# Kernel tuning notes

Measured on AMD Instinct MI355X. Metric: run time of the kernel, lower is better.

The kernel has to match this reference:

```python
import jax, jax.numpy as jnp
import numpy as np

H, KV, D, HID, FF = 32, 8, 128, 4096, 14336
EPS = 1e-5
ROPE_THETA = 1e9


def setup_inputs() -> dict:
    key = jax.random.key(0)
    ks = jax.random.split(key, 10)
    B, S = 1, 2048
    s = 0.02
    return {
        "hidden_states": jax.random.normal(ks[0], (B, S, HID), dtype=jnp.float32),
        "wq": jax.random.normal(ks[1], (HID, H * D), dtype=jnp.float32) * s,
        "wk": jax.random.normal(ks[2], (HID, KV * D), dtype=jnp.float32) * s,
        "wv": jax.random.normal(ks[3], (HID, KV * D), dtype=jnp.float32) * s,
        "wo": jax.random.normal(ks[4], (H * D, HID), dtype=jnp.float32) * s,
        "w_gate": jax.random.normal(ks[5], (HID, FF), dtype=jnp.float32) * s,
        "w_up": jax.random.normal(ks[6], (HID, FF), dtype=jnp.float32) * s,
        "w_down": jax.random.normal(ks[7], (FF, HID), dtype=jnp.float32) * s,
        "ln1_w": jnp.ones((HID,), dtype=jnp.float32),
        "ln2_w": jnp.ones((HID,), dtype=jnp.float32),
        "position_ids": jnp.arange(B * S, dtype=jnp.int32).reshape(B, S),
    }


def _rmsnorm(x, w):
    var = jnp.mean(jnp.square(x), axis=-1, keepdims=True)
    return x * jax.lax.rsqrt(var + EPS) * w


def _rope_cos_sin(position_ids):
    inv_freq = 1.0 / (ROPE_THETA ** (jnp.arange(0, D, 2, dtype=jnp.float32) / D))  # [D/2]
    ang = position_ids.astype(jnp.float32)[..., None] * inv_freq  # [B,S,D/2]
    ang = jnp.concatenate([ang, ang], axis=-1)  # [B,S,D]
    return jnp.cos(ang), jnp.sin(ang)


def _rotate_half(x):
    x1, x2 = x[..., : D // 2], x[..., D // 2:]
    return jnp.concatenate([-x2, x1], axis=-1)


def _apply_rope(x, cos, sin):
    # x: [B,S,h,D]; cos/sin: [B,S,D]
    c, s = cos[:, :, None, :], sin[:, :, None, :]
    return x * c + _rotate_half(x) * s


def reference(hidden_states, wq, wk, wv, wo, w_gate, w_up, w_down, ln1_w, ln2_w, position_ids):
    B, S, _ = hidden_states.shape
    G = H // KV  # query groups per kv head

    # --- attention block ---
    residual = hidden_states
    x = _rmsnorm(hidden_states, ln1_w)
    q = (x @ wq).reshape(B, S, H, D)
    k = (x @ wk).reshape(B, S, KV, D)
    v = (x @ wv).reshape(B, S, KV, D)

    cos, sin = _rope_cos_sin(position_ids)
    q = _apply_rope(q, cos, sin)
    k = _apply_rope(k, cos, sin)

    # GQA: group query heads over kv heads, [B,S,KV,G,D]
    qg = q.reshape(B, S, KV, G, D)
    scores = jnp.einsum("bqhgd,bkhd->bhgqk", qg, k) / jnp.sqrt(jnp.float32(D))
    causal = position_ids[:, :, None] >= position_ids[:, None, :]  # [B,S,S]
    scores = jnp.where(causal[:, None, None, :, :], scores, jnp.float32(-1e9))
    probs = jax.nn.softmax(scores, axis=-1)
    attn = jnp.einsum("bhgqk,bkhd->bqhgd", probs, v).reshape(B, S, H * D)
    hidden_states = residual + attn @ wo

    # --- MLP block (SwiGLU) ---
    residual = hidden_states
    x = _rmsnorm(hidden_states, ln2_w)
    mlp = (jax.nn.silu(x @ w_gate) * (x @ w_up)) @ w_down
    return residual + mlp
```

## Files before the change

kernel.cpp:

```cpp
#include <hip/hip_runtime.h>

typedef short bf16x8 __attribute__((ext_vector_type(8)));
typedef float f32x4 __attribute__((ext_vector_type(4)));

#define DEV __device__ __forceinline__

constexpr int SEQ = 2048;
constexpr int HID = 4096;
constexpr int NH  = 32;
constexpr int NKV = 8;
constexpr int DH  = 128;
constexpr int FF  = 14336;
constexpr int QKVN = NH * DH + 2 * NKV * DH;

DEV unsigned short f2bf(float f) {
  union { float f; unsigned u; } x; x.f = f;
  unsigned r = x.u + 0x7fffu + ((x.u >> 16) & 1u);
  return (unsigned short)(r >> 16);
}
DEV float bf2f(unsigned short u) {
  union { unsigned u; float f; } x; x.u = ((unsigned)u) << 16; return x.f;
}
DEV void gload16(const void* g, void* l) {
  __builtin_amdgcn_global_load_lds(
      (const __attribute__((address_space(1))) unsigned*)g,
      (__attribute__((address_space(3))) unsigned*)l, 16, 0, 0);
}

__global__ __launch_bounds__(256) void rmsnorm_kernel(
    const float* __restrict__ x, const float* __restrict__ w,
    unsigned short* __restrict__ out) {
  const int row = blockIdx.x;
  const int tid = threadIdx.x;
  const float* xr = x + (size_t)row * HID;
  float4 v[4];
  float ss = 0.f;
#pragma unroll
  for (int i = 0; i < 4; ++i) {
    v[i] = *(const float4*)(xr + i * 1024 + tid * 4);
    ss += v[i].x * v[i].x + v[i].y * v[i].y + v[i].z * v[i].z + v[i].w * v[i].w;
  }
#pragma unroll
  for (int m = 1; m < 64; m <<= 1) ss += __shfl_xor(ss, m);
  __shared__ float red[4];
  if ((tid & 63) == 0) red[tid >> 6] = ss;
  __syncthreads();
  float tot = red[0] + red[1] + red[2] + red[3];
  float rms = rsqrtf(tot / (float)HID + 1e-5f);
  unsigned short* orow = out + (size_t)row * HID;
#pragma unroll
  for (int i = 0; i < 4; ++i) {
    int base = i * 1024 + tid * 4;
    ushort4 o;
    o.x = f2bf(v[i].x * rms * w[base + 0]);
    o.y = f2bf(v[i].y * rms * w[base + 1]);
    o.z = f2bf(v[i].z * rms * w[base + 2]);
    o.w = f2bf(v[i].w * rms * w[base + 3]);
    *(ushort4*)(orow + base) = o;
  }
}

__global__ __launch_bounds__(256) void wtrans_kernel(
    const float* __restrict__ W, unsigned short* __restrict__ WT, int K,
    int N) {
  __shared__ unsigned short t[64][72];
  const int k0 = blockIdx.x * 64, n0 = blockIdx.y * 64;
  const int tid = threadIdx.x;
  const int tk = tid >> 4;
  const int tn4 = (tid & 15) * 4;
#pragma unroll
  for (int p = 0; p < 4; ++p) {
    int k = tk + p * 16;
    float4 v = *(const float4*)(W + (size_t)(k0 + k) * N + n0 + tn4);
    t[tn4 + 0][k] = f2bf(v.x);
    t[tn4 + 1][k] = f2bf(v.y);
    t[tn4 + 2][k] = f2bf(v.z);
    t[tn4 + 3][k] = f2bf(v.w);
  }
  __syncthreads();
#pragma unroll
  for (int p = 0; p < 4; ++p) {
    int n = tk + p * 16;
    ushort4 o = *(const ushort4*)&t[n][tn4];
    *(ushort4*)(WT + (size_t)(n0 + n) * K + k0 + tn4) = o;
  }
}

__global__ __launch_bounds__(256) void rope_kernel(unsigned short* __restrict__ x,
                                                   int nheads, int ld) {
  const int gid = blockIdx.x * 256 + threadIdx.x;
  const int i = gid & 63;
  const int t = gid >> 6;
  const int s = t / nheads;
  const int hh = t - s * nheads;
  float ang = (float)s * exp2f((float)i * (-29.897352853986263f / 64.f));
  float sn, cs;
  sincosf(ang, &sn, &cs);
  size_t base = (size_t)s * ld + hh * DH + i;
  float x1 = bf2f(x[base]);
  float x2 = bf2f(x[base + 64]);
  x[base]      = f2bf(x1 * cs - x2 * sn);
  x[base + 64] = f2bf(x2 * cs + x1 * sn);
}

__global__ __launch_bounds__(256) void silu_mul_kernel(
    const unsigned short* __restrict__ g, const unsigned short* __restrict__ u,
    unsigned short* __restrict__ out) {
  const size_t idx = ((size_t)blockIdx.x * 256 + threadIdx.x) * 4;
  ushort4 gv = *(const ushort4*)(g + idx);
  ushort4 uv = *(const ushort4*)(u + idx);
  float gf[4] = {bf2f(gv.x), bf2f(gv.y), bf2f(gv.z), bf2f(gv.w)};
  float uf[4] = {bf2f(uv.x), bf2f(uv.y), bf2f(uv.z), bf2f(uv.w)};
  ushort4 o;
  unsigned short* op = (unsigned short*)&o;
#pragma unroll
  for (int j = 0; j < 4; ++j) {
    float sl = gf[j] / (1.f + __expf(-gf[j]));
    op[j] = f2bf(sl * uf[j]);
  }
  *(ushort4*)(out + idx) = o;
}

template <int WROWS, int EPI>
__global__ __launch_bounds__(512, 2) void gemm8p_kernel(
    const unsigned short* __restrict__ A, const unsigned short* __restrict__ BT,
    void* __restrict__ Cv, const float* __restrict__ res, int gridM, int N,
    int K) {
  constexpr int BM = 2 * WROWS;
  constexpr int MF = WROWS / 32;
  constexpr int H  = 2 + BM / 128;
  constexpr int ABYTES = BM * 128;
  constexpr int BUFBYTES = ABYTES + 32768;
  __shared__ __align__(128) char sm[2 * BUFBYTES];

  const int tid  = threadIdx.x;
  const int lane = tid & 63;
  const int wv   = tid >> 6;
  const int nwg = gridDim.x;
  const int b = blockIdx.x;
  const int logical = (b & 7) * (nwg >> 3) + (b >> 3);
  const int m0 = (logical % gridM) * BM;
  const int n0 = (logical / gridM) * 256;
  const int wm = (wv >> 2) * WROWS;
  const int wn = (wv & 3) * 64;
  const int nt = K >> 6;

  const int srow = tid >> 3;
  const int scolb = (tid & 7) * 16;
  const int sldsbase = wv * 1024;

  auto stage = [&](int h, int t) {
    const int buf = t & 1;
    const int kt = t * 64;
    char* ldsOp;
    const unsigned short* g;
    int grow0, rowBase;
    if (h < 2) {
      ldsOp = sm + buf * BUFBYTES + ABYTES; g = BT; grow0 = n0; rowBase = h * 128;
    } else {
      ldsOp = sm + buf * BUFBYTES;          g = A;  grow0 = m0; rowBase = (h - 2) * 128;
    }
#pragma unroll
    for (int r = 0; r < 2; ++r) {
      int row = rowBase + r * 64 + srow;
      const char* gp = (const char*)g + ((size_t)(grow0 + row) * K + kt) * 2 +
                       (scolb ^ ((row & 7) << 4));
      gload16(gp, ldsOp + rowBase * 128 + r * 8192 + sldsbase);
    }
  };

  const int kb0 = (lane >> 4) * 16;
  const int lrow = lane & 15;
  auto ldA = [&](const char* sA, int mh, int mf, int ks) {
    int row = wm + mh * (WROWS / 2) + mf * 16 + lrow;
    return *(const bf16x8*)(sA + ((row * 128 + kb0 + ks * 64) ^ ((row & 7) << 4)));
  };
  auto ldB = [&](const char* sB, int j, int ks) {
    int col = wn + (j >> 1) * 32 + (j & 1) * 16 + lrow;
    return *(const bf16x8*)(sB + ((col * 128 + kb0 + ks * 64) ^ ((col & 7) << 4)));
  };

  f32x4 acc[2 * MF][4] = {};

#pragma unroll
  for (int h = 0; h < H; ++h) stage(h, 0);
#pragma unroll
  for (int h = 0; h < H - 1; ++h) stage(h, 1);
  if (H == 4) asm volatile("s_waitcnt vmcnt(6)" ::: "memory");
  else        asm volatile("s_waitcnt vmcnt(4)" ::: "memory");
  __builtin_amdgcn_s_barrier();

  for (int t = 0; t < nt; ++t) {
    const char* sA = sm + (t & 1) * BUFBYTES;
    const char* sB = sA + ABYTES;
    bf16x8 a[MF][2], bb[4][2];

#pragma unroll
    for (int mf = 0; mf < MF; ++mf) {
      a[mf][0] = ldA(sA, 0, mf, 0);
      a[mf][1] = ldA(sA, 0, mf, 1);
    }
#pragma unroll
    for (int j = 0; j < 4; ++j) {
      bb[j][0] = ldB(sB, j, 0);
      bb[j][1] = ldB(sB, j, 1);
    }
    if (t + 1 < nt) stage(H - 1, t + 1);
    __builtin_amdgcn_sched_barrier(0);
    __builtin_amdgcn_s_barrier();
    __builtin_amdgcn_s_setprio(1);
#pragma unroll
    for (int mf = 0; mf < MF; ++mf)
#pragma unroll
      for (int nf = 0; nf < 2; ++nf)
#pragma unroll
        for (int ks = 0; ks < 2; ++ks)
          acc[mf][nf] = __builtin_amdgcn_mfma_f32_16x16x32_bf16(
              a[mf][ks], bb[nf][ks], acc[mf][nf], 0, 0, 0);
    __builtin_amdgcn_s_setprio(0);
    __builtin_amdgcn_sched_barrier(0);
    __builtin_amdgcn_s_barrier();

    if (t + 2 < nt) stage(0, t + 2);
    __builtin_amdgcn_sched_barrier(0);
    __builtin_amdgcn_s_barrier();
    __builtin_amdgcn_s_setprio(1);
#pragma unroll
    for (int mf = 0; mf < MF; ++mf)
#pragma unroll
      for (int nf = 0; nf < 2; ++nf)
#pragma unroll
        for (int ks = 0; ks < 2; ++ks)
          acc[mf][2 + nf] = __builtin_amdgcn_mfma_f32_16x16x32_bf16(
              a[mf][ks], bb[2 + nf][ks], acc[mf][2 + nf], 0, 0, 0);
    __builtin_amdgcn_s_setprio(0);
    __builtin_amdgcn_sched_barrier(0);
    __builtin_amdgcn_s_barrier();

#pragma unroll
    for (int mf = 0; mf < MF; ++mf) {
      a[mf][0] = ldA(sA, 1, mf, 0);
      a[mf][1] = ldA(sA, 1, mf, 1);
    }
    if (t + 2 < nt) stage(1, t + 2);
    __builtin_amdgcn_sched_barrier(0);
    __builtin_amdgcn_s_barrier();
    __builtin_amdgcn_s_setprio(1);
#pragma unroll
    for (int mf = 0; mf < MF; ++mf)
#pragma unroll
      for (int nf = 0; nf < 2; ++nf)
#pragma unroll
        for (int ks = 0; ks < 2; ++ks)
          acc[MF + mf][nf] = __builtin_amdgcn_mfma_f32_16x16x32_bf16(
              a[mf][ks], bb[nf][ks], acc[MF + mf][nf], 0, 0, 0);
    __builtin_amdgcn_s_setprio(0);
    __builtin_amdgcn_sched_barrier(0);
    __builtin_amdgcn_s_barrier();

    if (H == 4 && t + 2 < nt) stage(2, t + 2);
    if (t + 2 < nt) {
      if (H == 4) asm volatile("s_waitcnt vmcnt(6)" ::: "memory");
      else        asm volatile("s_waitcnt vmcnt(4)" ::: "memory");
    } else {
      asm volatile("s_waitcnt vmcnt(0)" ::: "memory");
    }
    __builtin_amdgcn_sched_barrier(0);
    __builtin_amdgcn_s_barrier();
    __builtin_amdgcn_s_setprio(1);
#pragma unroll
    for (int mf = 0; mf < MF; ++mf)
#pragma unroll
      for (int nf = 0; nf < 2; ++nf)
#pragma unroll
        for (int ks = 0; ks < 2; ++ks)
          acc[MF + mf][2 + nf] = __builtin_amdgcn_mfma_f32_16x16x32_bf16(
              a[mf][ks], bb[2 + nf][ks], acc[MF + mf][2 + nf], 0, 0, 0);
    __builtin_amdgcn_s_setprio(0);
    __builtin_amdgcn_sched_barrier(0);
    __builtin_amdgcn_s_barrier();
  }

  const int rb = (lane >> 4) * 4;
#pragma unroll
  for (int i = 0; i < 2 * MF; ++i) {
    const int mh = i / MF, mf = i % MF;
#pragma unroll
    for (int j = 0; j < 4; ++j) {
#pragma unroll
      for (int r = 0; r < 4; ++r) {
        size_t row = (size_t)(m0 + wm + mh * (WROWS / 2) + mf * 16 + rb + r);
        size_t col = (size_t)(n0 + wn + (j >> 1) * 32 + (j & 1) * 16 + lrow);
        float vv = acc[i][j][r];
        if (EPI == 0) {
          ((unsigned short*)Cv)[row * N + col] = f2bf(vv);
        } else {
          ((float*)Cv)[row * N + col] = vv + res[row * N + col];
        }
      }
    }
  }
}

__global__ __launch_bounds__(256, 2) void attn_kernel(
    const unsigned short* __restrict__ QKV, unsigned short* __restrict__ Ob) {
  __shared__ __align__(128) char sm[16384 * 3 + 8192];
  char* sQ = sm;
  char* sK = sm + 16384;
  char* sV = sm + 32768;
  char* sP = sm + 49152;
  const int tid  = threadIdx.x;
  const int lane = tid & 63;
  const int wv   = tid >> 6;
  const int qb0  = blockIdx.x * 64;
  const int h    = blockIdx.y;
  const int hkv  = h >> 2;
  const int rbase = (lane >> 4) * 4;
  const int cbase = lane & 15;
  const unsigned short* Qp = QKV + h * DH;
  const unsigned short* Kp = QKV + NH * DH + hkv * DH;
  const unsigned short* Vp = QKV + NH * DH + NKV * DH + hkv * DH;

  const int oQ   = wv * 1024 + lane * 16;
  const int rowQ = oQ >> 8;
  const int cQ   = oQ & 255;
#pragma unroll
  for (int i = 0; i < 4; ++i) {
    int row = rowQ + 16 * i;
    const char* gp = (const char*)Qp + ((size_t)(qb0 + row) * QKVN) * 2 +
                     (cQ ^ ((row & 15) << 4));
    gload16(gp, sQ + i * 4096 + wv * 1024);
  }

  f32x4 oacc[8] = {};
  float m_r[4] = {-1e30f, -1e30f, -1e30f, -1e30f};
  float l_r[4] = {0.f, 0.f, 0.f, 0.f};

  const int d4   = (tid & 31) * 4;
  const int kv2b = (tid >> 5) * 2;
  const int ntiles = blockIdx.x + 1;

  for (int t = 0; t < ntiles; ++t) {
    const int kt0 = t * 64;
    __syncthreads();
#pragma unroll
    for (int i = 0; i < 4; ++i) {
      int row = rowQ + 16 * i;
      const char* gp = (const char*)Kp + ((size_t)(kt0 + row) * QKVN) * 2 +
                       (cQ ^ ((row & 15) << 4));
      gload16(gp, sK + i * 4096 + wv * 1024);
    }
#pragma unroll
    for (int i = 0; i < 4; ++i) {
      int kv2 = kv2b + 16 * i;
      const unsigned short* g0 = Vp + (size_t)(kt0 + kv2) * QKVN + d4;
      ushort4 r0 = *(const ushort4*)g0;
      ushort4 r1 = *(const ushort4*)(g0 + QKVN);
      unsigned short a0[4] = {r0.x, r0.y, r0.z, r0.w};
      unsigned short a1[4] = {r1.x, r1.y, r1.z, r1.w};
#pragma unroll
      for (int j = 0; j < 4; ++j) {
        int dd = d4 + j;
        *(unsigned*)(sV + ((dd * 128 + kv2 * 2) ^ ((dd & 7) << 4))) =
            (unsigned)a0[j] | ((unsigned)a1[j] << 16);
      }
    }
    __syncthreads();

    f32x4 sacc[4] = {};
#pragma unroll
    for (int kk = 0; kk < 4; ++kk) {
      int kb = (lane >> 4) * 16 + kk * 64;
      int qrow = wv * 16 + (lane & 15);
      bf16x8 aq =
          *(const bf16x8*)(sQ + ((qrow * 256 + kb) ^ ((qrow & 15) << 4)));
#pragma unroll
      for (int ni = 0; ni < 4; ++ni) {
        int krow = ni * 16 + (lane & 15);
        bf16x8 bk =
            *(const bf16x8*)(sK + ((krow * 256 + kb) ^ ((krow & 15) << 4)));
        sacc[ni] =
            __builtin_amdgcn_mfma_f32_16x16x32_bf16(aq, bk, sacc[ni], 0, 0, 0);
      }
    }

    const float scale = 0.08838834764831845f;
#pragma unroll
    for (int r = 0; r < 4; ++r) {
      int qg = qb0 + wv * 16 + rbase + r;
      float mx = -1e30f;
#pragma unroll
      for (int ni = 0; ni < 4; ++ni) {
        int cg = kt0 + ni * 16 + cbase;
        float sv = sacc[ni][r] * scale;
        sv = (cg <= qg) ? sv : -1e30f;
        sacc[ni][r] = sv;
        mx = fmaxf(mx, sv);
      }
      mx = fmaxf(mx, __shfl_xor(mx, 1));
      mx = fmaxf(mx, __shfl_xor(mx, 2));
      mx = fmaxf(mx, __shfl_xor(mx, 4));
      mx = fmaxf(mx, __shfl_xor(mx, 8));
      float mnew = fmaxf(m_r[r], mx);
      float sf = __expf(m_r[r] - mnew);
      m_r[r] = mnew;
      float rsum = 0.f;
#pragma unroll
      for (int ni = 0; ni < 4; ++ni) {
        float pv = __expf(sacc[ni][r] - mnew);
        sacc[ni][r] = pv;
        rsum += pv;
      }
      rsum += __shfl_xor(rsum, 1);
      rsum += __shfl_xor(rsum, 2);
      rsum += __shfl_xor(rsum, 4);
      rsum += __shfl_xor(rsum, 8);
      l_r[r] = l_r[r] * sf + rsum;
#pragma unroll
      for (int nt = 0; nt < 8; ++nt) oacc[nt][r] *= sf;
    }

    char* pw = sP + wv * 2048;
#pragma unroll
    for (int ni = 0; ni < 4; ++ni)
#pragma unroll
      for (int r = 0; r < 4; ++r) {
        int row = rbase + r;
        int cb2 = (ni * 16 + cbase) * 2;
        *(unsigned short*)(pw + ((row * 128 + cb2) ^ ((row & 7) << 4))) =
            f2bf(sacc[ni][r]);
      }
    asm volatile("s_waitcnt lgkmcnt(0)" ::: "memory");

#pragma unroll
    for (int kk = 0; kk < 2; ++kk) {
      int kb = (lane >> 4) * 16 + kk * 64;
      int prow = lane & 15;
      bf16x8 ap =
          *(const bf16x8*)(pw + ((prow * 128 + kb) ^ ((prow & 7) << 4)));
#pragma unroll
      for (int nt = 0; nt < 8; ++nt) {
        int vrow = nt * 16 + (lane & 15);
        bf16x8 bv =
            *(const bf16x8*)(sV + ((vrow * 128 + kb) ^ ((vrow & 7) << 4)));
        oacc[nt] =
            __builtin_amdgcn_mfma_f32_16x16x32_bf16(ap, bv, oacc[nt], 0, 0, 0);
      }
    }
  }

#pragma unroll
  for (int nt = 0; nt < 8; ++nt)
#pragma unroll
    for (int r = 0; r < 4; ++r) {
      size_t row = (size_t)(qb0 + wv * 16 + rbase + r);
      int col = nt * 16 + cbase;
      Ob[row * (NH * DH) + h * DH + col] = f2bf(oacc[nt][r] / l_r[r]);
    }
}

extern "C" void kernel_launch(void* const* d_in, const int* in_sizes, int n_in,
                              void* d_out, int out_size, void* d_ws,
                              size_t ws_size, hipStream_t stream) {
  const float* hs  = (const float*)d_in[0];
  const float* wq  = (const float*)d_in[1];
  const float* wk  = (const float*)d_in[2];
  const float* wvp = (const float*)d_in[3];
  const float* wo  = (const float*)d_in[4];
  const float* wg  = (const float*)d_in[5];
  const float* wu  = (const float*)d_in[6];
  const float* wd  = (const float*)d_in[7];
  const float* ln1 = (const float*)d_in[8];
  const float* ln2 = (const float*)d_in[9];

  char* p = (char*)d_ws;
  size_t need = 0;
  auto alloc = [&](size_t bytes) {
    char* r = p + need;
    need += (bytes + 255) & ~(size_t)255;
    return r;
  };
  unsigned short* T1   = (unsigned short*)alloc((size_t)FF * HID * 2);
  unsigned short* xn   = (unsigned short*)alloc((size_t)SEQ * HID * 2);
  unsigned short* qkv  = (unsigned short*)alloc((size_t)SEQ * QKVN * 2);
  unsigned short* ab   = (unsigned short*)alloc((size_t)SEQ * NH * DH * 2);
  float*          h2   = (float*)alloc((size_t)SEQ * HID * 4);
  unsigned short* xn2  = (unsigned short*)alloc((size_t)SEQ * HID * 2);
  unsigned short* gbuf = (unsigned short*)alloc((size_t)SEQ * FF * 2);
  unsigned short* ubuf = (unsigned short*)alloc((size_t)SEQ * FF * 2);
  if (need > ws_size) return;

  rmsnorm_kernel<<<SEQ, 256, 0, stream>>>(hs, ln1, xn);
  wtrans_kernel<<<dim3(HID / 64, HID / 64), 256, 0, stream>>>(wq, T1, HID, HID);
  wtrans_kernel<<<dim3(HID / 64, (NKV * DH) / 64), 256, 0, stream>>>(
      wk, T1 + (size_t)(NH * DH) * HID, HID, NKV * DH);
  wtrans_kernel<<<dim3(HID / 64, (NKV * DH) / 64), 256, 0, stream>>>(
      wvp, T1 + (size_t)(NH * DH + NKV * DH) * HID, HID, NKV * DH);
  gemm8p_kernel<128, 0><<<(SEQ / 256) * (QKVN / 256), 512, 0, stream>>>(
      xn, T1, qkv, nullptr, SEQ / 256, QKVN, HID);
  rope_kernel<<<(SEQ * NH * 64) / 256, 256, 0, stream>>>(qkv, NH, QKVN);
  rope_kernel<<<(SEQ * NKV * 64) / 256, 256, 0, stream>>>(qkv + NH * DH, NKV,
                                                          QKVN);
  attn_kernel<<<dim3(SEQ / 64, NH), 256, 0, stream>>>(qkv, ab);
  wtrans_kernel<<<dim3(HID / 64, HID / 64), 256, 0, stream>>>(wo, T1, HID, HID);
  gemm8p_kernel<64, 1><<<(SEQ / 128) * (HID / 256), 512, 0, stream>>>(
      ab, T1, h2, hs, SEQ / 128, HID, HID);
  rmsnorm_kernel<<<SEQ, 256, 0, stream>>>(h2, ln2, xn2);
  wtrans_kernel<<<dim3(HID / 64, FF / 64), 256, 0, stream>>>(wg, T1, HID, FF);
  gemm8p_kernel<128, 0><<<(SEQ / 256) * (FF / 256), 512, 0, stream>>>(
      xn2, T1, gbuf, nullptr, SEQ / 256, FF, HID);
  wtrans_kernel<<<dim3(HID / 64, FF / 64), 256, 0, stream>>>(wu, T1, HID, FF);
  gemm8p_kernel<128, 0><<<(SEQ / 256) * (FF / 256), 512, 0, stream>>>(
      xn2, T1, ubuf, nullptr, SEQ / 256, FF, HID);
  silu_mul_kernel<<<((size_t)SEQ * FF) / 1024, 256, 0, stream>>>(gbuf, ubuf,
                                                                 gbuf);
  wtrans_kernel<<<dim3(FF / 64, HID / 64), 256, 0, stream>>>(wd, T1, FF, HID);
  gemm8p_kernel<64, 1><<<(SEQ / 128) * (HID / 256), 512, 0, stream>>>(
      gbuf, T1, d_out, h2, SEQ / 128, HID, FF);
}
```

Before: 1.436 ms.

## Double-buffer K/V tiles in attention, enlarge query tile, schedule heavy blocks first

The attention kernel now processes 128 query rows per block with 8 waves and double-buffers the K and V tiles in shared memory. The next tile's loads are issued before the current tile's compute, which removes one barrier per iteration. Q fragments are kept in registers instead of being reloaded from LDS each tile. Blocks are launched on a 1D grid ordered so the longest causal rows run first, to reduce tail imbalance. The cost is more LDS per block, which limits occupancy to one block per CU, and more registers held for the prefetched V.

```diff
diff --git a/kernel.cpp b/kernel.cpp
--- a/kernel.cpp
+++ b/kernel.cpp
@@ -302,85 +302,116 @@
   }
 }
 
-__global__ __launch_bounds__(256, 2) void attn_kernel(
+__global__ __launch_bounds__(512, 1) void attn_kernel(
     const unsigned short* __restrict__ QKV, unsigned short* __restrict__ Ob) {
-  __shared__ __align__(128) char sm[16384 * 3 + 8192];
-  char* sQ = sm;
-  char* sK = sm + 16384;
-  char* sV = sm + 32768;
-  char* sP = sm + 49152;
+  __shared__ __align__(128) char sm[114688];
+  char* sQ  = sm;
+  char* sK0 = sm + 32768;
+  char* sK1 = sm + 49152;
+  char* sV0 = sm + 65536;
+  char* sV1 = sm + 81920;
+  char* sP  = sm + 98304;
   const int tid  = threadIdx.x;
   const int lane = tid & 63;
   const int wv   = tid >> 6;
-  const int qb0  = blockIdx.x * 64;
-  const int h    = blockIdx.y;
-  const int hkv  = h >> 2;
+  const int logical = blockIdx.x;
+  const int xr = 15 - (logical >> 5);
+  const int h = logical & 31;
+  const int qb0 = xr * 128;
+  const int hkv = h >> 2;
   const int rbase = (lane >> 4) * 4;
   const int cbase = lane & 15;
   const unsigned short* Qp = QKV + h * DH;
   const unsigned short* Kp = QKV + NH * DH + hkv * DH;
   const unsigned short* Vp = QKV + NH * DH + NKV * DH + hkv * DH;
 
-  const int oQ   = wv * 1024 + lane * 16;
-  const int rowQ = oQ >> 8;
-  const int cQ   = oQ & 255;
 #pragma unroll
   for (int i = 0; i < 4; ++i) {
-    int row = rowQ + 16 * i;
+    int offs = i * 8192 + tid * 16;
+    int row = offs >> 8, col = offs & 255;
     const char* gp = (const char*)Qp + ((size_t)(qb0 + row) * QKVN) * 2 +
-                     (cQ ^ ((row & 15) << 4));
-    gload16(gp, sQ + i * 4096 + wv * 1024);
+                     (col ^ ((row & 15) << 4));
+    gload16(gp, sQ + i * 8192 + wv * 1024);
+  }
+
+  auto stageK = [&](int t) {
+    char* dst = (t & 1) ? sK1 : sK0;
+    const int kt0 = t * 64;
+#pragma unroll
+    for (int i = 0; i < 2; ++i) {
+      int offs = i * 8192 + tid * 16;
+      int row = offs >> 8, col = offs & 255;
+      const char* gp = (const char*)Kp + ((size_t)(kt0 + row) * QKVN) * 2 +
+                       (col ^ ((row & 15) << 4));
+      gload16(gp, dst + i * 8192 + wv * 1024);
+    }
+  };
+
+  const int d4  = (tid & 31) * 4;
+  const int kv4 = (tid >> 5) * 4;
+  const int rot = (tid >> 1) & 3;
+  auto loadV = [&](int t, ushort4* vr) {
+    const unsigned short* g0 = Vp + (size_t)(t * 64 + kv4) * QKVN + d4;
+#pragma unroll
+    for (int k = 0; k < 4; ++k) vr[k] = *(const ushort4*)(g0 + (size_t)k * QKVN);
+  };
+  auto writeV = [&](int t, const ushort4* vr) {
+    char* dst = (t & 1) ? sV1 : sV0;
+    const unsigned short* a0 = (const unsigned short*)&vr[0];
+    const unsigned short* a1 = (const unsigned short*)&vr[1];
+    const unsigned short* a2 = (const unsigned short*)&vr[2];
+    const unsigned short* a3 = (const unsigned short*)&vr[3];
+#pragma unroll
+    for (int j = 0; j < 4; ++j) {
+      int jj = (j + rot) & 3;
+      int dd = d4 + jj;
+      uint2 pk;
+      pk.x = (unsigned)a0[jj] | ((unsigned)a1[jj] << 16);
+      pk.y = (unsigned)a2[jj] | ((unsigned)a3[jj] << 16);
+      *(uint2*)(dst + ((dd * 128 + kv4 * 2) ^ ((dd & 7) << 4))) = pk;
+    }
+  };
+
+  ushort4 vr[4];
+  stageK(0);
+  loadV(0, vr);
+  asm volatile("s_waitcnt vmcnt(0)" ::: "memory");
+  writeV(0, vr);
+  __syncthreads();
+
+  const int qrow = wv * 16 + (lane & 15);
+  bf16x8 aq[4];
+#pragma unroll
+  for (int kk = 0; kk < 4; ++kk) {
+    int kb = (lane >> 4) * 16 + kk * 64;
+    aq[kk] = *(const bf16x8*)(sQ + ((qrow * 256 + kb) ^ ((qrow & 15) << 4)));
   }
 
   f32x4 oacc[8] = {};
   float m_r[4] = {-1e30f, -1e30f, -1e30f, -1e30f};
   float l_r[4] = {0.f, 0.f, 0.f, 0.f};
-
-  const int d4   = (tid & 31) * 4;
-  const int kv2b = (tid >> 5) * 2;
-  const int ntiles = blockIdx.x + 1;
+  const int ntiles = 2 * (xr + 1);
 
   for (int t = 0; t < ntiles; ++t) {
     const int kt0 = t * 64;
-    __syncthreads();
-#pragma unroll
-    for (int i = 0; i < 4; ++i) {
-      int row = rowQ + 16 * i;
-      const char* gp = (const char*)Kp + ((size_t)(kt0 + row) * QKVN) * 2 +
-                       (cQ ^ ((row & 15) << 4));
-      gload16(gp, sK + i * 4096 + wv * 1024);
-    }
-#pragma unroll
-    for (int i = 0; i < 4; ++i) {
-      int kv2 = kv2b + 16 * i;
-      const unsigned short* g0 = Vp + (size_t)(kt0 + kv2) * QKVN + d4;
-      ushort4 r0 = *(const ushort4*)g0;
-      ushort4 r1 = *(const ushort4*)(g0 + QKVN);
-      unsigned short a0[4] = {r0.x, r0.y, r0.z, r0.w};
-      unsigned short a1[4] = {r1.x, r1.y, r1.z, r1.w};
-#pragma unroll
-      for (int j = 0; j < 4; ++j) {
-        int dd = d4 + j;
-        *(unsigned*)(sV + ((dd * 128 + kv2 * 2) ^ ((dd & 7) << 4))) =
-            (unsigned)a0[j] | ((unsigned)a1[j] << 16);
-      }
-    }
-    __syncthreads();
+    const char* cK = (t & 1) ? sK1 : sK0;
+    const char* cV = (t & 1) ? sV1 : sV0;
+    if (t + 1 < ntiles) {
+      stageK(t + 1);
+      loadV(t + 1, vr);
+    }
 
     f32x4 sacc[4] = {};
 #pragma unroll
     for (int kk = 0; kk < 4; ++kk) {
       int kb = (lane >> 4) * 16 + kk * 64;
-      int qrow = wv * 16 + (lane & 15);
-      bf16x8 aq =
-          *(const bf16x8*)(sQ + ((qrow * 256 + kb) ^ ((qrow & 15) << 4)));
 #pragma unroll
       for (int ni = 0; ni < 4; ++ni) {
         int krow = ni * 16 + (lane & 15);
         bf16x8 bk =
-            *(const bf16x8*)(sK + ((krow * 256 + kb) ^ ((krow & 15) << 4)));
-        sacc[ni] =
-            __builtin_amdgcn_mfma_f32_16x16x32_bf16(aq, bk, sacc[ni], 0, 0, 0);
+            *(const bf16x8*)(cK + ((krow * 256 + kb) ^ ((krow & 15) << 4)));
+        sacc[ni] = __builtin_amdgcn_mfma_f32_16x16x32_bf16(aq[kk], bk,
+                                                           sacc[ni], 0, 0, 0);
       }
     }
 
@@ -417,7 +448,7 @@
       rsum += __shfl_xor(rsum, 8);
       l_r[r] = l_r[r] * sf + rsum;
 #pragma unroll
-      for (int nt = 0; nt < 8; ++nt) oacc[nt][r] *= sf;
+      for (int nt2 = 0; nt2 < 8; ++nt2) oacc[nt2][r] *= sf;
     }
 
     char* pw = sP + wv * 2048;
@@ -439,23 +470,29 @@
       bf16x8 ap =
           *(const bf16x8*)(pw + ((prow * 128 + kb) ^ ((prow & 7) << 4)));
 #pragma unroll
-      for (int nt = 0; nt < 8; ++nt) {
-        int vrow = nt * 16 + (lane & 15);
+      for (int nt2 = 0; nt2 < 8; ++nt2) {
+        int vrow = nt2 * 16 + (lane & 15);
         bf16x8 bv =
-            *(const bf16x8*)(sV + ((vrow * 128 + kb) ^ ((vrow & 7) << 4)));
-        oacc[nt] =
-            __builtin_amdgcn_mfma_f32_16x16x32_bf16(ap, bv, oacc[nt], 0, 0, 0);
+            *(const bf16x8*)(cV + ((vrow * 128 + kb) ^ ((vrow & 7) << 4)));
+        oacc[nt2] =
+            __builtin_amdgcn_mfma_f32_16x16x32_bf16(ap, bv, oacc[nt2], 0, 0, 0);
       }
     }
-  }
-
-#pragma unroll
-  for (int nt = 0; nt < 8; ++nt)
+
+    if (t + 1 < ntiles) {
+      asm volatile("s_waitcnt vmcnt(0)" ::: "memory");
+      writeV(t + 1, vr);
+    }
+    __syncthreads();
+  }
+
+#pragma unroll
+  for (int nt2 = 0; nt2 < 8; ++nt2)
 #pragma unroll
     for (int r = 0; r < 4; ++r) {
       size_t row = (size_t)(qb0 + wv * 16 + rbase + r);
-      int col = nt * 16 + cbase;
-      Ob[row * (NH * DH) + h * DH + col] = f2bf(oacc[nt][r] / l_r[r]);
+      int col = nt2 * 16 + cbase;
+      Ob[row * (NH * DH) + h * DH + col] = f2bf(oacc[nt2][r] / l_r[r]);
     }
 }
 
@@ -501,7 +538,7 @@
   rope_kernel<<<(SEQ * NH * 64) / 256, 256, 0, stream>>>(qkv, NH, QKVN);
   rope_kernel<<<(SEQ * NKV * 64) / 256, 256, 0, stream>>>(qkv + NH * DH, NKV,
                                                           QKVN);
-  attn_kernel<<<dim3(SEQ / 64, NH), 256, 0, stream>>>(qkv, ab);
+  attn_kernel<<<512, 512, 0, stream>>>(qkv, ab);
   wtrans_kernel<<<dim3(HID / 64, HID / 64), 256, 0, stream>>>(wo, T1, HID, HID);
   gemm8p_kernel<64, 1><<<(SEQ / 128) * (HID / 256), 512, 0, stream>>>(
       ab, T1, h2, hs, SEQ / 128, HID, HID);
```

Result: faster. 1.301 ms (-9.4%).
